# Optimization experiments

Measured on AMD Instinct MI355X. Metric: run time of the kernel, lower is better.

## Reference

```python
import jax, jax.numpy as jnp
import numpy as np
from jax import lax

HEADS = 8
DIM_HEAD = 64
SCALE = DIM_HEAD ** -0.5

def conv2d(x, w, stride=1, pad=0):
    return lax.conv_general_dilated(
        x, w, window_strides=(stride, stride),
        padding=[(pad, pad), (pad, pad)],
        dimension_numbers=("NCHW", "OIHW", "NCHW"))

def setup_inputs() -> dict:
    key = jax.random.key(0)
    ks = jax.random.split(key, 5)
    b, dim, H, W = 8, 256, 32, 32
    inner = HEADS * DIM_HEAD  # 512
    x = jax.random.normal(ks[0], (b, dim, H, W), jnp.float32)
    Wq = jax.random.normal(ks[1], (inner, dim, 1, 1), jnp.float32) * 0.05
    Wkv = jax.random.normal(ks[2], (2 * inner, dim, 3, 3), jnp.float32) * 0.05
    Wout = jax.random.normal(ks[3], (dim, inner, 1, 1), jnp.float32) * 0.05
    bout = jnp.zeros((dim,), jnp.float32)
    return {"x": x, "Wq": Wq, "Wkv": Wkv, "Wout": Wout, "bout": bout}

def reference(x, Wq, Wkv, Wout, bout):
    b = x.shape[0]
    h, d = HEADS, DIM_HEAD
    q = conv2d(x, Wq, stride=1, pad=0)        # [b, h*d, H, W]
    kv = conv2d(x, Wkv, stride=1, pad=1)      # [b, 2*h*d, H, W]
    k, v = jnp.split(kv, 2, axis=1)
    out_h, out_w = q.shape[-2:]

    def to_bhnd(t):
        # b (h d) x y -> b h (x y) d
        B, _, X, Y = t.shape
        return t.reshape(B, h, d, X * Y).transpose(0, 1, 3, 2)

    q, k, v = map(to_bhnd, (q, k, v))
    dots = jnp.einsum("bhid,bhjd->bhij", q, k) * SCALE
    attn = jax.nn.softmax(dots, axis=-1)
    out = jnp.einsum("bhij,bhjd->bhid", attn, v)  # [b, h, n, d]
    # b h (x y) d -> b (h d) x y
    out = out.transpose(0, 1, 3, 2).reshape(b, h * d, out_h, out_w)
    out = jax.nn.gelu(out, approximate=False)
    out = conv2d(out, Wout, stride=1, pad=0) + bout[None, :, None, None]
    return out
```

## Files before the change

### kernel.cpp

```cpp
#include <hip/hip_runtime.h>
#include <math.h>

#define BATCH 8
#define DIM   256
#define NPIX  1024
#define DHEAD 64
#define INNER 512
#define KVCH  1024
#define PPIX  1156

typedef _Float16 half8 __attribute__((ext_vector_type(8)));
typedef _Float16 half4 __attribute__((ext_vector_type(4)));
typedef float    f32x4 __attribute__((ext_vector_type(4)));
typedef float    f32x16 __attribute__((ext_vector_type(16)));
#define MFMA16(a, b, c) __builtin_amdgcn_mfma_f32_16x16x32_f16(a, b, c, 0, 0, 0)
#define MFMA32(a, b, c) __builtin_amdgcn_mfma_f32_32x32x16_f16(a, b, c, 0, 0, 0)

static __device__ __forceinline__ float gelu_f(float v) {
    return 0.5f * v * (1.0f + erff(v * 0.70710678118654752440f));
}

static __device__ __forceinline__ void gload16(const _Float16* g, _Float16* l) {
    __builtin_amdgcn_global_load_lds(
        (const __attribute__((address_space(1))) unsigned int*)g,
        (__attribute__((address_space(3))) unsigned int*)l, 16, 0, 0);
}

__global__ __launch_bounds__(256) void prep_kernel(
    const float* __restrict__ Wq, const float* __restrict__ Wkv,
    const float* __restrict__ Wout, const float* __restrict__ x,
    _Float16* __restrict__ Aq, _Float16* __restrict__ Akv,
    _Float16* __restrict__ Aout, _Float16* __restrict__ xtp)
{
    const int bid = blockIdx.x, tid = threadIdx.x;
    if (bid < 512) {
        __shared__ float ts[64][65];
        const int pt = (bid & 15) * 64, ic0 = ((bid >> 4) & 3) * 64, b = bid >> 6;
        const float* xb = x + (((size_t)(b * DIM + ic0)) << 10) + pt;
#pragma unroll
        for (int e = tid; e < 4096; e += 256) {
            int i = e >> 6, p = e & 63;
            ts[i][p] = xb[((size_t)i << 10) + p];
        }
        __syncthreads();
#pragma unroll
        for (int e = tid; e < 512; e += 256) {
            int p = e >> 3, ig = e & 7;
            int gp = pt + p, y = gp >> 5, xc = gp & 31;
            half8 v;
#pragma unroll
            for (int u = 0; u < 8; ++u) v[u] = (_Float16)ts[ig * 8 + u][p];
            *(half8*)&xtp[((size_t)b * PPIX + (y + 1) * 34 + xc + 1) * 256 + ic0 + ig * 8] = v;
        }
    } else if (bid < 10752) {
        const int e = (bid - 512) * 256 + tid;
        if (e < 131072) Aq[e] = (_Float16)Wq[e];
        const int e2 = e - 131072;
        if (e2 >= 0 && e2 < 2359296) {
            int oc = e2 / 2304, r = e2 - oc * 2304;
            int s = r >> 8, ic = r & 255;
            Akv[e2] = (_Float16)Wkv[oc * 2304 + ic * 9 + s];
        }
        const int e3 = e - 131072 - 2359296;
        if (e3 >= 0 && e3 < 131072) Aout[e3] = (_Float16)Wout[e3];
    } else {
        const int he = (bid - 10752) * 256 + tid;
        if (he < 270336) {
            int b = he / 33792;
            int r = he - b * 33792;
            int hp = r >> 8, ic = r & 255;
            int row, col;
            if (hp < 34)      { row = 0;  col = hp; }
            else if (hp < 68) { row = 33; col = hp - 34; }
            else { int k2 = hp - 68; row = 1 + (k2 >> 1); col = (k2 & 1) * 33; }
            xtp[((size_t)b * PPIX + row * 34 + col) * 256 + ic] = (_Float16)0.f;
        }
    }
}

__global__ __launch_bounds__(256) void qkv_gemm_kernel(
    const _Float16* __restrict__ Akv, const _Float16* __restrict__ Aq,
    const _Float16* __restrict__ xtp, _Float16* __restrict__ qt,
    _Float16* __restrict__ ktp, _Float16* __restrict__ vb)
{
    __shared__ _Float16 As[128 * 64];
    __shared__ _Float16 Bs[128 * 64];
    const int nt = blockIdx.x, mt = blockIdx.y, b = blockIdx.z;
    const bool QBLK = (mt >= 8);
    const int tid = threadIdx.x;
    const int w = tid >> 6, lane = tid & 63;
    const int l31 = lane & 31, kh = lane >> 5;
    const int m0 = (QBLK ? mt - 8 : mt) * 128, p0 = nt * 128;
    const int wm = (w >> 1) * 64, wn = (w & 1) * 64;

    const int srow = lane >> 3;
    const int scol = ((lane & 7) ^ srow) * 8;

    const _Float16* abase = QBLK ? Aq : Akv;
    const int astride = QBLK ? 256 : 2304;
    const int ktend = QBLK ? 4 : 36;

    const _Float16* agp[4];
    const _Float16* bgp[4];
#pragma unroll
    for (int c = 0; c < 4; ++c) {
        int row = (w * 4 + c) * 8 + srow;
        agp[c] = abase + (size_t)(m0 + row) * astride + scol;
        int p = p0 + row, py = p >> 5, px = p & 31;
        bgp[c] = xtp + ((size_t)b * PPIX + (py + 1) * 34 + px + 1) * 256 + scol;
    }

    f32x16 acc[2][2];
#pragma unroll
    for (int mf = 0; mf < 2; ++mf)
#pragma unroll
        for (int nf = 0; nf < 2; ++nf)
#pragma unroll
            for (int r = 0; r < 16; ++r) acc[mf][nf][r] = 0.f;

    for (int kt = 0; kt < ktend; ++kt) {
        __syncthreads();
        const int s = QBLK ? 4 : (kt >> 2);
        const int doff = (s / 3 - 1) * 34 + (s - (s / 3) * 3) - 1;
        const int boff = doff * 256 + (kt & 3) * 64;
#pragma unroll
        for (int c = 0; c < 4; ++c)
            gload16(agp[c] + kt * 64, &As[(w * 4 + c) * 512]);
#pragma unroll
        for (int c = 0; c < 4; ++c)
            gload16(bgp[c] + boff, &Bs[(w * 4 + c) * 512]);
        __syncthreads();
#pragma unroll
        for (int kc = 0; kc < 4; ++kc) {
            const int cx = ((((kc << 1) | kh) ^ (l31 & 7)) << 3);
            half8 af[2], bf[2];
#pragma unroll
            for (int mf = 0; mf < 2; ++mf)
                af[mf] = *(const half8*)&As[(wm + mf * 32 + l31) * 64 + cx];
#pragma unroll
            for (int nf = 0; nf < 2; ++nf)
                bf[nf] = *(const half8*)&Bs[(wn + nf * 32 + l31) * 64 + cx];
#pragma unroll
            for (int mf = 0; mf < 2; ++mf)
#pragma unroll
                for (int nf = 0; nf < 2; ++nf)
                    acc[mf][nf] = MFMA32(af[mf], bf[nf], acc[mf][nf]);
        }
    }

#pragma unroll
    for (int mf = 0; mf < 2; ++mf) {
        const int mbase = m0 + wm + mf * 32;
        if (!QBLK && mbase >= 512) {
#pragma unroll
            for (int nf = 0; nf < 2; ++nf) {
                const int pix = p0 + wn + nf * 32 + l31;
#pragma unroll
                for (int reg = 0; reg < 16; ++reg) {
                    const int mv = mbase - 512 + (reg & 3) + 8 * (reg >> 2) + 4 * kh;
                    vb[(((size_t)(b * 512 + mv)) << 10) + pix] =
                        (_Float16)acc[mf][nf][reg];
                }
            }
        } else {
            const int h = mbase >> 6;
            const int dbase = (mbase & 63) + kh * 4;
            _Float16* dst = QBLK ? qt : ktp;
#pragma unroll
            for (int nf = 0; nf < 2; ++nf) {
                const int pix = p0 + wn + nf * 32 + l31;
#pragma unroll
                for (int g = 0; g < 4; ++g) {
                    half4 v4;
#pragma unroll
                    for (int r = 0; r < 4; ++r) {
                        float vv = acc[mf][nf][g * 4 + r];
                        if (QBLK) vv *= 0.125f;
                        v4[r] = (_Float16)vv;
                    }
                    *(half4*)&dst[((((size_t)(b * 8 + h)) << 10) + pix) * 64 + dbase + g * 8] = v4;
                }
            }
        }
    }
}

template<int M, int K, int KROW>
__global__ __launch_bounds__(256) void out_gemm_kernel(
    const _Float16* __restrict__ A, const _Float16* __restrict__ act,
    float* __restrict__ Cout, const float* __restrict__ bias)
{
    __shared__ _Float16 As[128 * 64];
    __shared__ _Float16 Bs[64 * 64];
    const int nt = blockIdx.x, mt = blockIdx.y, b = blockIdx.z;
    const int tid = threadIdx.x;
    const int w = tid >> 6, lane = tid & 63;
    const int quad = lane >> 4, l15 = lane & 15;
    const int m0 = mt * 128, p0 = nt * 64;
    const int wm = w * 32;
    const f32x4 Z4 = {0.f, 0.f, 0.f, 0.f};

    const int srow = lane >> 3;
    const int scol = ((lane & 7) ^ srow) * 8;

    const _Float16* agp[4];
#pragma unroll
    for (int c = 0; c < 4; ++c) {
        int row = (w * 4 + c) * 8 + srow;
        agp[c] = A + (size_t)(m0 + row) * K + scol;
    }
    const _Float16* bgp[2];
#pragma unroll
    for (int c = 0; c < 2; ++c) {
        int row = (w * 2 + c) * 8 + srow;
        bgp[c] = act + (size_t)(b * NPIX + p0 + row) * KROW + scol;
    }

    f32x4 acc[2][4];
#pragma unroll
    for (int mi = 0; mi < 2; ++mi)
#pragma unroll
        for (int ni = 0; ni < 4; ++ni) acc[mi][ni] = Z4;

    for (int kt = 0; kt < K / 64; ++kt) {
        __syncthreads();
#pragma unroll
        for (int c = 0; c < 4; ++c)
            gload16(agp[c] + kt * 64, &As[(w * 4 + c) * 512]);
#pragma unroll
        for (int c = 0; c < 2; ++c)
            gload16(bgp[c] + kt * 64, &Bs[(w * 2 + c) * 512]);
        __syncthreads();
#pragma unroll
        for (int ks = 0; ks < 2; ++ks) {
            half8 av[2], bv[4];
#pragma unroll
            for (int mi = 0; mi < 2; ++mi) {
                const int r = wm + mi * 16 + l15;
                av[mi] = *(const half8*)&As[r * 64 + (((ks * 4 + quad) ^ (l15 & 7)) << 3)];
            }
#pragma unroll
            for (int ni = 0; ni < 4; ++ni) {
                const int r = ni * 16 + l15;
                bv[ni] = *(const half8*)&Bs[r * 64 + (((ks * 4 + quad) ^ (l15 & 7)) << 3)];
            }
#pragma unroll
            for (int mi = 0; mi < 2; ++mi)
#pragma unroll
                for (int ni = 0; ni < 4; ++ni)
                    acc[mi][ni] = MFMA16(av[mi], bv[ni], acc[mi][ni]);
        }
    }

#pragma unroll
    for (int mi = 0; mi < 2; ++mi) {
#pragma unroll
        for (int r = 0; r < 4; ++r) {
            const int m = m0 + wm + mi * 16 + quad * 4 + r;
            const float bv = bias[m];
#pragma unroll
            for (int ni = 0; ni < 4; ++ni) {
                const int pix = p0 + ni * 16 + l15;
                Cout[(((size_t)(b * M + m)) << 10) + pix] = acc[mi][ni][r] + bv;
            }
        }
    }
}

__global__ __launch_bounds__(256) void attn_kernel(
    const _Float16* __restrict__ qt,
    const _Float16* __restrict__ ktp,
    const _Float16* __restrict__ vbb,
    _Float16* __restrict__ gout)
{
    __shared__ _Float16 Ks[128 * 64];
    __shared__ _Float16 Vs[64 * 128];
    __shared__ _Float16 Pb[128 * 128];
    const int qtile = blockIdx.x, bh = blockIdx.y;
    const int b = bh >> 3, h = bh & 7;
    const int p0 = qtile * 128;
    const int tid = threadIdx.x;
    const int w = tid >> 6, lane = tid & 63;
    const int quad = lane >> 4, l15 = lane & 15;
    const f32x4 Z4 = {0.f, 0.f, 0.f, 0.f};

    half8 ones;
#pragma unroll
    for (int u = 0; u < 8; ++u) ones[u] = (_Float16)1.0f;

    half8 qf[2][2];
    {
        const _Float16* qrow =
            qt + ((((size_t)(bh)) << 10) + p0 + w * 32 + l15) * 64;
#pragma unroll
        for (int iff = 0; iff < 2; ++iff)
#pragma unroll
            for (int ks = 0; ks < 2; ++ks)
                qf[iff][ks] = *(const half8*)(qrow + iff * 16 * 64 + ks * 32 + quad * 8);
    }

    const _Float16* kbase = ktp + ((size_t)bh << 16);
    const _Float16* vbase = vbb + (((size_t)(b * 512 + h * 64)) << 10);

    f32x4 oacc[4][2];
#pragma unroll
    for (int mf = 0; mf < 4; ++mf)
#pragma unroll
        for (int iff = 0; iff < 2; ++iff) oacc[mf][iff] = Z4;
    f32x4 racc[2] = {Z4, Z4};

    const int kchunk = (lane & 7) ^ (lane >> 3);
    for (int kt = 0; kt < 8; ++kt) {
        const int pk = kt * 128;
        __syncthreads();
        const _Float16* kg = kbase + (size_t)pk * 64;
#pragma unroll
        for (int i = 0; i < 4; ++i) {
            const int t = i * 4 + w;
            gload16(kg + (t * 8 + (lane >> 3)) * 64 + kchunk * 8, &Ks[t * 512]);
        }
#pragma unroll
        for (int i = 0; i < 4; ++i) {
            const int t = i * 4 + w;
            const int vd = t * 4 + (lane >> 4);
            gload16(vbase + ((size_t)vd << 10) + pk + (((lane & 15) ^ (vd & 15)) << 3),
                    &Vs[t * 512]);
        }
        __syncthreads();

#pragma unroll
        for (int g = 0; g < 2; ++g) {
            f32x4 s[4][2];
#pragma unroll
            for (int jf2 = 0; jf2 < 4; ++jf2) {
                const int jr = (g * 4 + jf2) * 16 + l15;
                const half8 ka0 = *(const half8*)&Ks[jr * 64 + ((quad ^ (l15 & 7)) << 3)];
                const half8 ka1 = *(const half8*)&Ks[jr * 64 + (((4 + quad) ^ (l15 & 7)) << 3)];
#pragma unroll
                for (int iff = 0; iff < 2; ++iff) {
                    s[jf2][iff] = MFMA16(ka0, qf[iff][0], Z4);
                    s[jf2][iff] = MFMA16(ka1, qf[iff][1], s[jf2][iff]);
                }
            }
#pragma unroll
            for (int jf2 = 0; jf2 < 4; ++jf2) {
#pragma unroll
                for (int iff = 0; iff < 2; ++iff) {
                    half4 pv4;
#pragma unroll
                    for (int r = 0; r < 4; ++r)
                        pv4[r] = (_Float16)__expf(s[jf2][iff][r] - 8.0f);
                    const int i = w * 32 + iff * 16 + l15;
                    const int c = ((g * 4 + jf2) << 1) + (quad >> 1);
                    *(half4*)&Pb[i * 128 + ((c ^ l15) << 3) + ((quad & 1) << 2)] = pv4;
                }
            }
        }
#pragma unroll
        for (int kc = 0; kc < 4; ++kc) {
            half8 bv[2];
#pragma unroll
            for (int iff = 0; iff < 2; ++iff) {
                const int i = w * 32 + iff * 16 + l15;
                bv[iff] = *(const half8*)&Pb[i * 128 + (((kc * 4 + quad) ^ l15) << 3)];
                racc[iff] = MFMA16(ones, bv[iff], racc[iff]);
            }
#pragma unroll
            for (int mf = 0; mf < 4; ++mf) {
                const int vr = mf * 16 + l15;
                const half8 va = *(const half8*)&Vs[vr * 128 + (((kc * 4 + quad) ^ l15) << 3)];
#pragma unroll
                for (int iff = 0; iff < 2; ++iff)
                    oacc[mf][iff] = MFMA16(va, bv[iff], oacc[mf][iff]);
            }
        }
    }

    float rinv[2];
#pragma unroll
    for (int iff = 0; iff < 2; ++iff) rinv[iff] = 1.f / racc[iff][0];

    __syncthreads();
    _Float16* scr = Pb;
#pragma unroll
    for (int mf = 0; mf < 4; ++mf) {
#pragma unroll
        for (int iff = 0; iff < 2; ++iff) {
            half4 o4;
#pragma unroll
            for (int r = 0; r < 4; ++r)
                o4[r] = (_Float16)gelu_f(oacc[mf][iff][r] * rinv[iff]);
            const int i = w * 32 + iff * 16 + l15;
            *(half4*)&scr[i * 72 + mf * 16 + quad * 4] = o4;
        }
    }
    __syncthreads();
    _Float16* go = gout + ((size_t)(b * NPIX + p0)) * INNER + h * 64;
#pragma unroll
    for (int it = 0; it < 4; ++it) {
        const int e = tid + it * 256;
        const int p = e >> 3, dg = e & 7;
        *(half8*)(go + (size_t)p * INNER + dg * 8) = *(const half8*)&scr[p * 72 + dg * 8];
    }
}

extern "C" void kernel_launch(void* const* d_in, const int* in_sizes, int n_in,
                              void* d_out, int out_size, void* d_ws, size_t ws_size,
                              hipStream_t stream)
{
    const float* x    = (const float*)d_in[0];
    const float* Wq   = (const float*)d_in[1];
    const float* Wkv  = (const float*)d_in[2];
    const float* Wout = (const float*)d_in[3];
    const float* bout = (const float*)d_in[4];
    float* out = (float*)d_out;

    _Float16* xtp  = (_Float16*)d_ws;
    _Float16* Aq   = xtp  + (size_t)BATCH * PPIX * DIM;
    _Float16* Akv  = Aq   + (size_t)INNER * DIM;
    _Float16* Aout = Akv  + (size_t)KVCH * 2304;
    _Float16* qt   = Aout + (size_t)DIM * INNER;
    _Float16* vb   = qt   + (size_t)BATCH * NPIX * INNER;
    _Float16* ktp  = vb   + (size_t)BATCH * NPIX * INNER;
    _Float16* gout = ktp  + (size_t)BATCH * NPIX * INNER;

    prep_kernel<<<11808, 256, 0, stream>>>(Wq, Wkv, Wout, x, Aq, Akv, Aout, xtp);
    qkv_gemm_kernel<<<dim3(8, 12, BATCH), 256, 0, stream>>>(Akv, Aq, xtp, qt, ktp, vb);
    attn_kernel<<<dim3(8, 64), 256, 0, stream>>>(qt, ktp, vb, gout);
    out_gemm_kernel<DIM, 512, 512>
        <<<dim3(16, 2, BATCH), 256, 0, stream>>>(Aout, gout, out, bout);
}
```

Measured before the change: 176.0 us.

## Double-buffer LDS in QKV GEMM and widen pixel tile to 256

Converts the QKV conv-GEMM main loop to double-buffered shared memory, issuing the next k-tile's global-to-LDS loads before computing on the current one, with a single barrier per iteration. It also doubles the pixel tile per block from 128 to 256, giving each warp 2x4 MFMA fragments and halving the grid. This aims to hide load latency and improve operand reuse, at the cost of much more LDS (96KB), more accumulator registers and fewer blocks (384), which may reduce occupancy.

```diff
diff --git a/kernel.cpp b/kernel.cpp
--- a/kernel.cpp
+++ b/kernel.cpp
@@ -83,15 +83,15 @@
     const _Float16* __restrict__ xtp, _Float16* __restrict__ qt,
     _Float16* __restrict__ ktp, _Float16* __restrict__ vb)
 {
-    __shared__ _Float16 As[128 * 64];
-    __shared__ _Float16 Bs[128 * 64];
+    __shared__ _Float16 As[2][128 * 64];
+    __shared__ _Float16 Bs[2][256 * 64];
     const int nt = blockIdx.x, mt = blockIdx.y, b = blockIdx.z;
     const bool QBLK = (mt >= 8);
     const int tid = threadIdx.x;
     const int w = tid >> 6, lane = tid & 63;
     const int l31 = lane & 31, kh = lane >> 5;
-    const int m0 = (QBLK ? mt - 8 : mt) * 128, p0 = nt * 128;
-    const int wm = (w >> 1) * 64, wn = (w & 1) * 64;
+    const int m0 = (QBLK ? mt - 8 : mt) * 128, p0 = nt * 256;
+    const int wm = (w >> 1) * 64, wn = (w & 1) * 128;
 
     const int srow = lane >> 3;
     const int scol = ((lane & 7) ^ srow) * 8;
@@ -101,51 +101,71 @@
     const int ktend = QBLK ? 4 : 36;
 
     const _Float16* agp[4];
-    const _Float16* bgp[4];
+    const _Float16* bgp[8];
 #pragma unroll
     for (int c = 0; c < 4; ++c) {
         int row = (w * 4 + c) * 8 + srow;
         agp[c] = abase + (size_t)(m0 + row) * astride + scol;
+    }
+#pragma unroll
+    for (int c = 0; c < 8; ++c) {
+        int row = (w * 8 + c) * 8 + srow;
         int p = p0 + row, py = p >> 5, px = p & 31;
         bgp[c] = xtp + ((size_t)b * PPIX + (py + 1) * 34 + px + 1) * 256 + scol;
     }
 
-    f32x16 acc[2][2];
+    f32x16 acc[2][4];
 #pragma unroll
     for (int mf = 0; mf < 2; ++mf)
 #pragma unroll
-        for (int nf = 0; nf < 2; ++nf)
+        for (int nf = 0; nf < 4; ++nf)
 #pragma unroll
             for (int r = 0; r < 16; ++r) acc[mf][nf][r] = 0.f;
 
+    {
+        const int s0 = QBLK ? 4 : 0;
+        const int doff0 = (s0 / 3 - 1) * 34 + (s0 - (s0 / 3) * 3) - 1;
+        const int boff0 = doff0 * 256;
+#pragma unroll
+        for (int c = 0; c < 4; ++c)
+            gload16(agp[c], &As[0][(w * 4 + c) * 512]);
+#pragma unroll
+        for (int c = 0; c < 8; ++c)
+            gload16(bgp[c] + boff0, &Bs[0][(w * 8 + c) * 512]);
+    }
+    __syncthreads();
+
     for (int kt = 0; kt < ktend; ++kt) {
-        __syncthreads();
-        const int s = QBLK ? 4 : (kt >> 2);
-        const int doff = (s / 3 - 1) * 34 + (s - (s / 3) * 3) - 1;
-        const int boff = doff * 256 + (kt & 3) * 64;
-#pragma unroll
-        for (int c = 0; c < 4; ++c)
-            gload16(agp[c] + kt * 64, &As[(w * 4 + c) * 512]);
-#pragma unroll
-        for (int c = 0; c < 4; ++c)
-            gload16(bgp[c] + boff, &Bs[(w * 4 + c) * 512]);
-        __syncthreads();
+        const int cur = kt & 1;
+        if (kt + 1 < ktend) {
+            const int kn = kt + 1;
+            const int s = QBLK ? 4 : (kn >> 2);
+            const int doff = (s / 3 - 1) * 34 + (s - (s / 3) * 3) - 1;
+            const int boff = doff * 256 + (kn & 3) * 64;
+#pragma unroll
+            for (int c = 0; c < 4; ++c)
+                gload16(agp[c] + kn * 64, &As[cur ^ 1][(w * 4 + c) * 512]);
+#pragma unroll
+            for (int c = 0; c < 8; ++c)
+                gload16(bgp[c] + boff, &Bs[cur ^ 1][(w * 8 + c) * 512]);
+        }
 #pragma unroll
         for (int kc = 0; kc < 4; ++kc) {
             const int cx = ((((kc << 1) | kh) ^ (l31 & 7)) << 3);
-            half8 af[2], bf[2];
+            half8 af[2], bf[4];
 #pragma unroll
             for (int mf = 0; mf < 2; ++mf)
-                af[mf] = *(const half8*)&As[(wm + mf * 32 + l31) * 64 + cx];
-#pragma unroll
-            for (int nf = 0; nf < 2; ++nf)
-                bf[nf] = *(const half8*)&Bs[(wn + nf * 32 + l31) * 64 + cx];
+                af[mf] = *(const half8*)&As[cur][(wm + mf * 32 + l31) * 64 + cx];
+#pragma unroll
+            for (int nf = 0; nf < 4; ++nf)
+                bf[nf] = *(const half8*)&Bs[cur][(wn + nf * 32 + l31) * 64 + cx];
 #pragma unroll
             for (int mf = 0; mf < 2; ++mf)
 #pragma unroll
-                for (int nf = 0; nf < 2; ++nf)
+                for (int nf = 0; nf < 4; ++nf)
                     acc[mf][nf] = MFMA32(af[mf], bf[nf], acc[mf][nf]);
         }
+        __syncthreads();
     }
 
 #pragma unroll
@@ -153,7 +173,7 @@
         const int mbase = m0 + wm + mf * 32;
         if (!QBLK && mbase >= 512) {
 #pragma unroll
-            for (int nf = 0; nf < 2; ++nf) {
+            for (int nf = 0; nf < 4; ++nf) {
                 const int pix = p0 + wn + nf * 32 + l31;
 #pragma unroll
                 for (int reg = 0; reg < 16; ++reg) {
@@ -167,7 +187,7 @@
             const int dbase = (mbase & 63) + kh * 4;
             _Float16* dst = QBLK ? qt : ktp;
 #pragma unroll
-            for (int nf = 0; nf < 2; ++nf) {
+            for (int nf = 0; nf < 4; ++nf) {
                 const int pix = p0 + wn + nf * 32 + l31;
 #pragma unroll
                 for (int g = 0; g < 4; ++g) {
@@ -425,7 +445,7 @@
     _Float16* gout = ktp  + (size_t)BATCH * NPIX * INNER;
 
     prep_kernel<<<11808, 256, 0, stream>>>(Wq, Wkv, Wout, x, Aq, Akv, Aout, xtp);
-    qkv_gemm_kernel<<<dim3(8, 12, BATCH), 256, 0, stream>>>(Akv, Aq, xtp, qt, ktp, vb);
+    qkv_gemm_kernel<<<dim3(4, 12, BATCH), 256, 0, stream>>>(Akv, Aq, xtp, qt, ktp, vb);
     attn_kernel<<<dim3(8, 64), 256, 0, stream>>>(qt, ktp, vb, gout);
     out_gemm_kernel<DIM, 512, 512>
         <<<dim3(16, 2, BATCH), 256, 0, stream>>>(Aout, gout, out, bout);
```

Measured after the change: 198.3 us. +12.7%, slower.
